# Kernel tuning notes

Hardware: AMD Instinct MI355X
Metric: run time of the kernel (lower is better)

The kernel has to match this reference:

```python
import jax, jax.numpy as jnp
import numpy as np

CUTOFF = 8.0  # SMEAMConfig.cutoff


def _natural_cubic_coeffs(t, y):
    """Natural cubic spline coefficients. t: [K] knots, y: [K, 1] values.
    Returns per-interval (a, b, c, d), each [K-1, 1]."""
    h = t[1:] - t[:-1]                              # [K-1]
    dy = (y[1:] - y[:-1]) / h[:, None]              # [K-1, 1]
    rhs = 6.0 * (dy[1:] - dy[:-1])                  # [K-2, 1]
    main = 2.0 * (h[:-1] + h[1:])
    A = jnp.diag(main) + jnp.diag(h[1:-1], 1) + jnp.diag(h[1:-1], -1)
    m_int = jnp.linalg.solve(A, rhs)                # interior second derivatives
    z = jnp.zeros((1, y.shape[1]), dtype=y.dtype)
    M = jnp.concatenate([z, m_int, z], axis=0)      # natural BC: M0 = M_{K-1} = 0
    a = y[:-1]
    b = dy - h[:, None] * (2.0 * M[:-1] + M[1:]) / 6.0
    c = M[:-1] / 2.0
    d = (M[1:] - M[:-1]) / (6.0 * h[:, None])
    return a, b, c, d


def _spline_eval(t, coeffs, x):
    """Evaluate spline at x: [T] -> [T, 1]. Edge intervals extrapolate."""
    a, b, c, d = coeffs
    idx = jnp.clip(jnp.searchsorted(t, x, side='right') - 1, 0, t.shape[0] - 2)
    s = (x - t[idx])[:, None]
    return a[idx] + s * (b[idx] + s * (c[idx] + s * d[idx]))


def setup_inputs() -> dict:
    key = jax.random.key(0)
    N, deg, K = 10000, 32, 7
    E = N * deg
    k1, k2, k3, k4 = jax.random.split(key, 4)
    # edge displacement vectors; scaled so bond lengths fall inside [0, cutoff]
    r = jax.random.normal(k1, (E, 3), dtype=jnp.float32) * 2.0
    f_coeffs = jax.random.uniform(k2, (K, 1), dtype=jnp.float32)
    g_coeffs = jax.random.uniform(k3, (K, 1), dtype=jnp.float32)
    src = jax.random.randint(k4, (E,), 0, N, dtype=jnp.int32)
    # fixed in-degree layout: edges with destination j are indices [j*deg, (j+1)*deg)
    dst = jnp.repeat(jnp.arange(N, dtype=jnp.int32), deg)
    return {"r": r, "f_coeffs": f_coeffs, "g_coeffs": g_coeffs,
            "src": src, "dst": dst, "deg": deg}


def reference(r, f_coeffs, g_coeffs, src, dst, deg):
    E = r.shape[0]
    K = f_coeffs.shape[0]
    knots_radial = jnp.linspace(0.0, CUTOFF, K, dtype=r.dtype)
    knots_angular = jnp.linspace(-1.0, 1.0, K, dtype=r.dtype)
    f_c = _natural_cubic_coeffs(knots_radial, f_coeffs)
    g_c = _natural_cubic_coeffs(knots_angular, g_coeffs)

    # line-graph (non-backtracking) triplets: e1 ends where e2 starts
    e2 = jnp.repeat(jnp.arange(E, dtype=jnp.int32), deg)                    # [T]
    e1 = (src[:, None] * deg + jnp.arange(deg, dtype=jnp.int32)).ravel()    # [T]
    valid = src[e1] != dst[e2]   # exclude backtracking e2 = reverse(e1)

    r1 = -r[e1]                  # [T, 3]
    r2 = r[e2]                   # [T, 3]
    l1 = jnp.linalg.norm(r1, axis=1)
    l2 = jnp.linalg.norm(r2, axis=1)
    bond_cosine = jnp.clip(jnp.sum(r1 * r2, axis=1) / (l1 * l2), -1.0, 1.0)

    m = (_spline_eval(knots_radial, f_c, l1)
         * _spline_eval(knots_radial, f_c, l2)
         * _spline_eval(knots_angular, g_c, bond_cosine))    # [T, 1]
    m = jnp.where(valid[:, None], m, jnp.zeros((), dtype=m.dtype))

    # scatter-sum triplet messages onto destination edges (line-graph nodes)
    ft = jax.ops.segment_sum(m, e2, num_segments=E)           # [E, 1]
    return ft
```

## Files before the change

kernel.cpp:

```cpp
#include <hip/hip_runtime.h>
#include <hip/hip_fp16.h>

#define DEG 32
#define K_KNOTS 7
#define NINT 6

typedef _Float16 half_t;
typedef _Float16 h2 __attribute__((ext_vector_type(2)));

union UF8 {
    uint2 u;
    struct { h2 xy; h2 zf; } h;
};

__device__ inline float fdot2(h2 a, h2 b, float c) {
#if __has_builtin(__builtin_amdgcn_fdot2)
    return __builtin_amdgcn_fdot2(a, b, c, false);
#else
    return (float)a.x * (float)b.x + (float)a.y * (float)b.y + c;
#endif
}

__device__ inline void spline_coeffs(const float* __restrict__ y, float h, float4* C) {
    float dy[NINT];
#pragma unroll
    for (int i = 0; i < NINT; ++i) dy[i] = (y[i + 1] - y[i]) / h;
    float rhs[5];
#pragma unroll
    for (int i = 0; i < 5; ++i) rhs[i] = 6.0f * (dy[i + 1] - dy[i]);
    float cp[5], dp[5];
    float denom = 4.0f * h;
    cp[0] = h / denom;
    dp[0] = rhs[0] / denom;
#pragma unroll
    for (int i = 1; i < 5; ++i) {
        denom = 4.0f * h - h * cp[i - 1];
        cp[i] = h / denom;
        dp[i] = (rhs[i] - h * dp[i - 1]) / denom;
    }
    float M[K_KNOTS];
    M[0] = 0.0f; M[6] = 0.0f;
    M[5] = dp[4];
#pragma unroll
    for (int i = 3; i >= 0; --i) M[i + 1] = dp[i] - cp[i] * M[i + 2];
#pragma unroll
    for (int i = 0; i < NINT; ++i) {
        C[i].x = y[i];
        C[i].y = dy[i] - h * (2.0f * M[i] + M[i + 1]) * (1.0f / 6.0f);
        C[i].z = M[i] * 0.5f;
        C[i].w = (M[i + 1] - M[i]) / (6.0f * h);
    }
}

__global__ __launch_bounds__(256) void edge_kernel(
    const float* __restrict__ r, const float* __restrict__ fc,
    uint2* __restrict__ uf, int E) {
    __shared__ float4 sF[NINT];
    if (threadIdx.x == 0) {
        float4 c[NINT];
        spline_coeffs(fc, 8.0f / 6.0f, c);
#pragma unroll
        for (int i = 0; i < NINT; ++i) sF[i] = c[i];
    }
    __syncthreads();
    int e = blockIdx.x * blockDim.x + threadIdx.x;
    if (e >= E) return;
    float x = r[3 * e + 0];
    float y = r[3 * e + 1];
    float z = r[3 * e + 2];
    float d = x * x + y * y + z * z;
    float rl = rsqrtf(d);
    float l = d * rl;
    float u = l * (6.0f / 8.0f);
    int idx = (int)u;
    idx = idx < 0 ? 0 : (idx > NINT - 1 ? NINT - 1 : idx);
    float s = l - (8.0f / 6.0f) * (float)idx;
    float4 c = sF[idx];
    float f = c.x + s * (c.y + s * (c.z + s * c.w));
    UF8 q;
    q.h.xy.x = (half_t)(x * rl);
    q.h.xy.y = (half_t)(y * rl);
    q.h.zf.x = (half_t)(z * rl);
    q.h.zf.y = (half_t)f;
    uf[e] = q.u;
}

__global__ __launch_bounds__(256) void triplet_kernel(
    const uint2* __restrict__ uf, const float* __restrict__ gc,
    const int* __restrict__ src, const int* __restrict__ dst,
    float* __restrict__ out, int E) {
    __shared__ float4 sG[NINT];
    if (threadIdx.x == 0) {
        float4 c[NINT];
        spline_coeffs(gc, 2.0f / 6.0f, c);
#pragma unroll
        for (int i = 0; i < NINT; ++i) sG[i] = c[i];
    }
    __syncthreads();

    int e = blockIdx.x * blockDim.x + threadIdx.x;
    if (e >= E) return;

    int a = src[e];
    int de = dst[e];
    UF8 qe; qe.u = uf[e];
    uint2 neg = qe.u;
    neg.x ^= 0x80008000u;
    neg.y ^= 0x00008000u;
    h2 ne_xy = __builtin_bit_cast(h2, neg.x);
    h2 ne_zf = __builtin_bit_cast(h2, neg.y);
    h2 ne_z0; ne_z0.x = ne_zf.x; ne_z0.y = (half_t)0.0f;
    float fe = (float)qe.h.zf.y;

    const uint4* blk = (const uint4*)(uf + (size_t)a * DEG);
    const int2* sblk = (const int2*)(src + (size_t)a * DEG);

    float acc = 0.0f;
#pragma unroll
    for (int it = 0; it < DEG / 2; ++it) {
        uint4 q = blk[it];
        int2 sp = sblk[it];
#pragma unroll
        for (int half = 0; half < 2; ++half) {
            h2 kxy = __builtin_bit_cast(h2, half ? q.z : q.x);
            h2 kzf = __builtin_bit_cast(h2, half ? q.w : q.y);
            int s2 = half ? sp.y : sp.x;
            float cosv = fdot2(kxy, ne_xy, fdot2(kzf, ne_z0, 0.0f));
            cosv = fminf(fmaxf(cosv, -1.0f), 1.0f);
            float u = (cosv + 1.0f) * 3.0f;
            int idx = (int)u;
            idx = idx > NINT - 1 ? NINT - 1 : idx;
            float s = cosv - (-1.0f + (2.0f / 6.0f) * (float)idx);
            float4 c = sG[idx];
            float g = c.x + s * (c.y + s * (c.z + s * c.w));
            float fk = (float)kzf.y;
            float term = (s2 != de) ? fk * g : 0.0f;
            acc += term;
        }
    }
    out[e] = fe * acc;
}

extern "C" void kernel_launch(void* const* d_in, const int* in_sizes, int n_in,
                              void* d_out, int out_size, void* d_ws, size_t ws_size,
                              hipStream_t stream) {
    const float* r   = (const float*)d_in[0];
    const float* fc  = (const float*)d_in[1];
    const float* gc  = (const float*)d_in[2];
    const int* src   = (const int*)d_in[3];
    const int* dst   = (const int*)d_in[4];
    float* out = (float*)d_out;
    int E = in_sizes[3];

    uint2* uf = (uint2*)d_ws;

    int threads = 256;
    int blocks1 = (E + threads - 1) / threads;
    edge_kernel<<<blocks1, threads, 0, stream>>>(r, fc, uf, E);

    int blocks2 = (E + threads - 1) / threads;
    triplet_kernel<<<blocks2, threads, 0, stream>>>(uf, gc, src, dst, out, E);
}
```

Baseline: 94.47 us.

## Split each edge's 32 triplets across four threads with shuffle reduction

The triplet kernel now assigns four lanes per destination edge, each handling 8 of the 32 incoming neighbor edges. Each lane issues all of its neighbor-record and src loads up front as wide vector loads, and the partial sums are combined with two xor shuffles. This raises parallelism and memory-level parallelism and spreads the per-edge gather latency across more threads. The cost is four times as many threads, redundant per-edge setup loads, and shuffle overhead.

```diff
diff --git a/kernel.cpp b/kernel.cpp
--- a/kernel.cpp
+++ b/kernel.cpp
@@ -98,7 +98,9 @@
     }
     __syncthreads();
 
-    int e = blockIdx.x * blockDim.x + threadIdx.x;
+    int t = blockIdx.x * blockDim.x + threadIdx.x;
+    int e = t >> 2;
+    int q = t & 3;
     if (e >= E) return;
 
     int a = src[e];
@@ -113,32 +115,41 @@
     float fe = (float)qe.h.zf.y;
 
     const uint4* blk = (const uint4*)(uf + (size_t)a * DEG);
-    const int2* sblk = (const int2*)(src + (size_t)a * DEG);
+    const int4* sblk = (const int4*)(src + (size_t)a * DEG);
+    uint4 rq[4];
+    int4 sq[2];
+#pragma unroll
+    for (int it = 0; it < 4; ++it) rq[it] = blk[q * 4 + it];
+#pragma unroll
+    for (int it = 0; it < 2; ++it) sq[it] = sblk[q * 2 + it];
 
     float acc = 0.0f;
 #pragma unroll
-    for (int it = 0; it < DEG / 2; ++it) {
-        uint4 q = blk[it];
-        int2 sp = sblk[it];
-#pragma unroll
-        for (int half = 0; half < 2; ++half) {
-            h2 kxy = __builtin_bit_cast(h2, half ? q.z : q.x);
-            h2 kzf = __builtin_bit_cast(h2, half ? q.w : q.y);
-            int s2 = half ? sp.y : sp.x;
-            float cosv = fdot2(kxy, ne_xy, fdot2(kzf, ne_z0, 0.0f));
-            cosv = fminf(fmaxf(cosv, -1.0f), 1.0f);
-            float u = (cosv + 1.0f) * 3.0f;
-            int idx = (int)u;
-            idx = idx > NINT - 1 ? NINT - 1 : idx;
-            float s = cosv - (-1.0f + (2.0f / 6.0f) * (float)idx);
-            float4 c = sG[idx];
-            float g = c.x + s * (c.y + s * (c.z + s * c.w));
-            float fk = (float)kzf.y;
-            float term = (s2 != de) ? fk * g : 0.0f;
-            acc += term;
-        }
+    for (int rr = 0; rr < 8; ++rr) {
+        uint4 qq = rq[rr >> 1];
+        unsigned w0 = (rr & 1) ? qq.z : qq.x;
+        unsigned w1 = (rr & 1) ? qq.w : qq.y;
+        int4 sv = sq[rr >> 2];
+        int s2 = (rr & 3) == 0 ? sv.x : (rr & 3) == 1 ? sv.y
+               : (rr & 3) == 2 ? sv.z : sv.w;
+        h2 kxy = __builtin_bit_cast(h2, w0);
+        h2 kzf = __builtin_bit_cast(h2, w1);
+        float cosv = fdot2(kxy, ne_xy, fdot2(kzf, ne_z0, 0.0f));
+        cosv = fminf(fmaxf(cosv, -1.0f), 1.0f);
+        float u = (cosv + 1.0f) * 3.0f;
+        int idx = (int)u;
+        idx = idx > NINT - 1 ? NINT - 1 : idx;
+        float s = cosv - (-1.0f + (2.0f / 6.0f) * (float)idx);
+        float4 c = sG[idx];
+        float g = c.x + s * (c.y + s * (c.z + s * c.w));
+        float fk = (float)kzf.y;
+        float term = (s2 != de) ? fk * g : 0.0f;
+        acc += term;
     }
-    out[e] = fe * acc;
+
+    acc += __shfl_xor(acc, 1, 64);
+    acc += __shfl_xor(acc, 2, 64);
+    if (q == 0) out[e] = fe * acc;
 }
 
 extern "C" void kernel_launch(void* const* d_in, const int* in_sizes, int n_in,
@@ -158,6 +169,7 @@
     int blocks1 = (E + threads - 1) / threads;
     edge_kernel<<<blocks1, threads, 0, stream>>>(r, fc, uf, E);
 
-    int blocks2 = (E + threads - 1) / threads;
+    long long T2 = (long long)E * 4;
+    int blocks2 = (int)((T2 + threads - 1) / threads);
     triplet_kernel<<<blocks2, threads, 0, stream>>>(uf, gc, src, dst, out, E);
 }
```

Result: faster. 82.05 us, median of 2 (-13.1%).
